# Optimization experiments

Measured on AMD Instinct MI355X. Metric: run time of the kernel, lower is better.

Reference implementation:

```python
import jax, jax.numpy as jnp
import numpy as np

B, N, E, D, H, L = 1, 50000, 800000, 128, 8, 3
HD = D // H
VOCAB = 7000
OUT = 10


def _ln(x, g, b, eps=1e-5):
    m = x.mean(-1, keepdims=True)
    v = ((x - m) ** 2).mean(-1, keepdims=True)
    return (x - m) * jax.lax.rsqrt(v + eps) * g + b


def setup_inputs() -> dict:
    key = jax.random.key(0)
    ks = jax.random.split(key, 40)
    std = 0.02 / np.sqrt(L)

    def w(k, shape):
        return (jax.random.normal(k, shape, jnp.float32) * std)

    inp = {
        "x_idx": jax.random.randint(ks[0], (B, N, 1), 0, VOCAB),
        "edge_index": jax.random.randint(ks[1], (2, E), 0, B * N),
        "emb": jax.random.normal(ks[2], (VOCAB, D), jnp.float32) * 0.02,
        # per-layer params stacked on leading L axis; linears stored [in, out]
        "Wq": w(ks[3], (L, D, D)), "bq": jnp.zeros((L, D), jnp.float32),
        "Wk": w(ks[4], (L, D, D)), "bk": jnp.zeros((L, D), jnp.float32),
        "Wv": w(ks[5], (L, D, D)), "bv": jnp.zeros((L, D), jnp.float32),
        "Wo": w(ks[6], (L, D, D)), "bo": jnp.zeros((L, D), jnp.float32),
        "g1": jnp.ones((L, D), jnp.float32), "be1": jnp.zeros((L, D), jnp.float32),
        "Wf1": w(ks[7], (L, D, 2 * D)), "bf1": jnp.zeros((L, 2 * D), jnp.float32),
        "Wf2": w(ks[8], (L, 2 * D, D)), "bf2": jnp.zeros((L, D), jnp.float32),
        "g2": jnp.ones((L, D), jnp.float32), "be2": jnp.zeros((L, D), jnp.float32),
        # MLPReadout: D -> D/2 -> D/4 -> OUT
        "mW0": w(ks[9], (D, D // 2)), "mb0": jnp.zeros((D // 2,), jnp.float32),
        "mW1": w(ks[10], (D // 2, D // 4)), "mb1": jnp.zeros((D // 4,), jnp.float32),
        "mW2": w(ks[11], (D // 4, OUT)), "mb2": jnp.zeros((OUT,), jnp.float32),
    }
    return inp


def reference(x_idx, edge_index, emb, Wq, bq, Wk, bk, Wv, bv, Wo, bo,
              g1, be1, Wf1, bf1, Wf2, bf2, g2, be2,
              mW0, mb0, mW1, mb1, mW2, mb2):
    # node embedding: sum over feature-index axis -> [B, N, D]
    x = emb[x_idx].sum(axis=-2)
    e0, e1 = edge_index[0], edge_index[1]
    scale = jnp.sqrt(jnp.float32(HD))

    for l in range(L):
        h = x
        hf = h.reshape(B * N, D)
        q = (hf @ Wq[l] + bq[l]).reshape(B * N, H, HD)
        k = (hf @ Wk[l] + bk[l]).reshape(B * N, H, HD)
        v = (hf @ Wv[l] + bv[l]).reshape(B * N, H, HD)
        # edge-indexed gather-mul-exp  [E, H, 1]
        score = jnp.clip(jnp.sum(k[e0] * q[e1], axis=-1, keepdims=True) / scale,
                         -5.0, 5.0)
        score = jnp.exp(score)
        msg = v[e0] * score                                    # [E, H, HD]
        wV = jax.ops.segment_sum(msg, e1, num_segments=B * N)  # [B*N, H, HD]
        Z = jax.ops.segment_sum(score, e1, num_segments=B * N) # [B*N, H, 1]
        attn = (wV / (Z + 1e-6)).reshape(B, N, D)
        y = attn @ Wo[l] + bo[l]
        x = _ln(h + y, g1[l], be1[l])
        # note: FFN input is y (attention output), per the original code
        y2 = jnp.maximum(y @ Wf1[l] + bf1[l], 0.0) @ Wf2[l] + bf2[l]
        x = _ln(x + y2, g2[l], be2[l])

    out = x.mean(axis=1)  # [B, D]
    out = jnp.maximum(out @ mW0 + mb0, 0.0)
    out = jnp.maximum(out @ mW1 + mb1, 0.0)
    return out @ mW2 + mb2  # [B, OUT]
```

## Files before the change

### kernel.cpp

```cpp
#include <hip/hip_runtime.h>
#include <hip/hip_bf16.h>

#define N_NODES 50000
#define N_EDGES 800000
#define DIM 128
#define NLAYERS 3

typedef short bf16x8 __attribute__((ext_vector_type(8)));
typedef float floatx4 __attribute__((ext_vector_type(4)));
typedef float floatx2 __attribute__((ext_vector_type(2)));

__device__ __forceinline__ unsigned short f2bf(float f) {
  unsigned int u = __builtin_bit_cast(unsigned int, f);
  return (unsigned short)((u + 0x7FFFu + ((u >> 16) & 1u)) >> 16);
}
__device__ __forceinline__ float bf2f(unsigned short h) {
  return __builtin_bit_cast(float, (unsigned int)h << 16);
}
__device__ __forceinline__ float2 bf2f2(unsigned int u) {
  float lo = __builtin_bit_cast(float, u << 16);
  float hi = __builtin_bit_cast(float, u & 0xFFFF0000u);
  return make_float2(lo, hi);
}

__global__ __launch_bounds__(256) void embed_kernel(
    const int* __restrict__ idx, const float* __restrict__ emb,
    unsigned short* __restrict__ xb)
{
  int gid = blockIdx.x * 256 + threadIdx.x;
  int n = gid >> 5;
  int c = (gid & 31) << 2;
  if (n >= N_NODES) return;
  int e = idx[n];
  float4 val = *(const float4*)(emb + (size_t)e * DIM + c);
  ushort4 pk;
  pk.x = f2bf(val.x); pk.y = f2bf(val.y); pk.z = f2bf(val.z); pk.w = f2bf(val.w);
  *(ushort4*)(xb + (size_t)n * DIM + c) = pk;
}

__global__ __launch_bounds__(256) void hist_kernel(
    const int* __restrict__ e1, int* __restrict__ counts,
    int* __restrict__ rank)
{
  int i = blockIdx.x * 256 + threadIdx.x;
  if (i < N_EDGES) rank[i] = atomicAdd(&counts[e1[i]], 1);
}

__global__ __launch_bounds__(256) void scan_local(
    const int* __restrict__ counts, int* __restrict__ offsets,
    int* __restrict__ bsums)
{
  __shared__ int buf[256];
  int t = threadIdx.x;
  int i = blockIdx.x * 256 + t;
  int v = (i < N_NODES) ? counts[i] : 0;
  buf[t] = v;
  __syncthreads();
  int s = v;
#pragma unroll
  for (int off = 1; off < 256; off <<= 1) {
    int t2 = (t >= off) ? buf[t - off] : 0;
    __syncthreads();
    s += t2;
    buf[t] = s;
    __syncthreads();
  }
  if (i < N_NODES) offsets[i] = s - v;
  if (t == 255) bsums[blockIdx.x] = s;
}

__global__ void scan_bsums(int* __restrict__ bsums, int nblk)
{
  __shared__ int buf[256];
  int t = threadIdx.x;
  int v = (t < nblk) ? bsums[t] : 0;
  buf[t] = v;
  __syncthreads();
  int s = v;
#pragma unroll
  for (int off = 1; off < 256; off <<= 1) {
    int t2 = (t >= off) ? buf[t - off] : 0;
    __syncthreads();
    s += t2;
    buf[t] = s;
    __syncthreads();
  }
  if (t < nblk) bsums[t] = s - v;
}

__global__ __launch_bounds__(256) void scan_add(
    int* __restrict__ offsets, const int* __restrict__ bsums)
{
  int i = blockIdx.x * 256 + threadIdx.x;
  if (i < N_NODES) offsets[i] += bsums[blockIdx.x];
  if (i == 0) offsets[N_NODES] = N_EDGES;
}

__global__ __launch_bounds__(256) void scatter_kernel(
    const int* __restrict__ e0, const int* __restrict__ e1,
    const int* __restrict__ offsets, const int* __restrict__ rank,
    int* __restrict__ csr)
{
  int i = blockIdx.x * 256 + threadIdx.x;
  if (i >= N_EDGES) return;
  csr[offsets[e1[i]] + rank[i]] = e0[i];
}

__global__ __launch_bounds__(256) void prep_all(
    const float* __restrict__ Wq, const float* __restrict__ Wk,
    const float* __restrict__ Wv, const float* __restrict__ Wo,
    const float* __restrict__ Wf1, const float* __restrict__ Wf2,
    unsigned short* __restrict__ wqkv, unsigned short* __restrict__ wo,
    unsigned short* __restrict__ wf1, unsigned short* __restrict__ wf2)
{
  int g = blockIdx.x * 256 + threadIdx.x;
  if (g < 18432) {
    int srcId = g / 6144; int rem = g - srcId * 6144;
    const float* W = (srcId == 0) ? Wq : (srcId == 1) ? Wk : Wv;
    int l = rem / 2048; int r2 = rem & 2047; int kq = r2 >> 7; int n = r2 & 127;
    const float* Wl = W + (size_t)l * 128 * 128;
    unsigned short* base = wqkv + (size_t)l * 128 * 384 + (size_t)(kq * 384 + srcId * 128 + n) * 8;
#pragma unroll
    for (int j = 0; j < 8; j++)
      base[j] = f2bf(Wl[(size_t)(kq * 8 + j) * 128 + n]);
    return;
  }
  g -= 18432;
  if (g < 6144) {
    int l = g / 2048; int r2 = g & 2047; int kq = r2 >> 7; int n = r2 & 127;
    const float* Wl = Wo + (size_t)l * 128 * 128;
    unsigned short* base = wo + (size_t)l * 128 * 128 + (size_t)(kq * 128 + n) * 8;
#pragma unroll
    for (int j = 0; j < 8; j++)
      base[j] = f2bf(Wl[(size_t)(kq * 8 + j) * 128 + n]);
    return;
  }
  g -= 6144;
  if (g < 12288) {
    int l = g / 4096; int r2 = g & 4095; int kq = r2 >> 8; int n = r2 & 255;
    const float* Wl = Wf1 + (size_t)l * 128 * 256;
    unsigned short* base = wf1 + (size_t)l * 128 * 256 + (size_t)(kq * 256 + n) * 8;
#pragma unroll
    for (int j = 0; j < 8; j++)
      base[j] = f2bf(Wl[(size_t)(kq * 8 + j) * 256 + n]);
    return;
  }
  g -= 12288;
  if (g < 12288) {
    int l = g / 4096; int r2 = g & 4095; int kq = r2 >> 7; int n = r2 & 127;
    const float* Wl = Wf2 + (size_t)l * 256 * 128;
    unsigned short* base = wf2 + (size_t)l * 256 * 128 + (size_t)(kq * 128 + n) * 8;
#pragma unroll
    for (int j = 0; j < 8; j++)
      base[j] = f2bf(Wl[(size_t)(kq * 8 + j) * 128 + n]);
  }
}

#define LSTR 136

__global__ __launch_bounds__(256) void qkv0_kernel(
    const unsigned short* __restrict__ xb,
    const unsigned short* __restrict__ wqkv,
    const float* __restrict__ bq, const float* __restrict__ bk,
    const float* __restrict__ bv,
    unsigned short* __restrict__ qkv, int nrows)
{
  __shared__ unsigned short XR[64 * LSTR];
  int tid = threadIdx.x;
  int wave = tid >> 6, lane = tid & 63;
  int quad = lane >> 4, l16 = lane & 15;
  int rbase = blockIdx.x * 64;
  int wrow = wave * 16;
  int rowg = min(rbase + wrow + l16, nrows - 1);
  int lrow_v = (wrow + l16) * LSTR + quad * 8;
  bool wr = (rbase + wrow + l16 < nrows);

  bf16x8 avQ[4];
  {
    const unsigned short* arow = xb + (size_t)rowg * 128 + quad * 8;
#pragma unroll
    for (int kb = 0; kb < 4; kb++)
      avQ[kb] = *(const bf16x8*)(arow + kb * 32);
  }
#pragma unroll
  for (int c = 0; c < 3; c++) {
    floatx4 accQ[8];
#pragma unroll
    for (int ct = 0; ct < 8; ct++) accQ[ct] = (floatx4)(0.f);
#pragma unroll
    for (int kb = 0; kb < 4; kb++) {
      int kq = kb * 4 + quad;
      bf16x8 bh[8];
#pragma unroll
      for (int ct = 0; ct < 8; ct++)
        bh[ct] = *(const bf16x8*)&wqkv[(size_t)(kq * 384 + c * 128 + ct * 16 + l16) * 8];
#pragma unroll
      for (int ct = 0; ct < 8; ct++)
        accQ[ct] = __builtin_amdgcn_mfma_f32_16x16x32_bf16(avQ[kb], bh[ct], accQ[ct], 0, 0, 0);
    }
    const float* bias = (c == 0) ? bq : (c == 1) ? bk : bv;
#pragma unroll
    for (int ct = 0; ct < 8; ct++) {
      float bvv = bias[ct * 16 + l16];
#pragma unroll
      for (int i = 0; i < 4; i++)
        XR[(wrow + quad * 4 + i) * LSTR + ct * 16 + l16] = f2bf(accQ[ct][i] + bvv);
    }
    if (wr) {
      if (c == 0) {
#pragma unroll
        for (int kb = 0; kb < 4; kb++)
          *(bf16x8*)&qkv[(size_t)(rbase + wrow + l16) * 256 + kb * 32 + quad * 8] =
              *(bf16x8*)&XR[lrow_v + kb * 32];
      } else {
#pragma unroll
        for (int kb = 0; kb < 4; kb++) {
          bf16x8 w = *(bf16x8*)&XR[lrow_v + kb * 32];
          int p0 = __builtin_amdgcn_cvt_pk_fp8_f32(
              bf2f((unsigned short)w[0]) * 8.f, bf2f((unsigned short)w[1]) * 8.f, 0, false);
          int p1 = __builtin_amdgcn_cvt_pk_fp8_f32(
              bf2f((unsigned short)w[2]) * 8.f, bf2f((unsigned short)w[3]) * 8.f, 0, false);
          int p2 = __builtin_amdgcn_cvt_pk_fp8_f32(
              bf2f((unsigned short)w[4]) * 8.f, bf2f((unsigned short)w[5]) * 8.f, 0, false);
          int p3 = __builtin_amdgcn_cvt_pk_fp8_f32(
              bf2f((unsigned short)w[6]) * 8.f, bf2f((unsigned short)w[7]) * 8.f, 0, false);
          int2 st;
          st.x = (p0 & 0xffff) | (p1 << 16);
          st.y = (p2 & 0xffff) | (p3 << 16);
          *(int2*)&qkv[(size_t)(rbase + wrow + l16) * 256 + 128 + (c - 1) * 64 +
                       kb * 16 + quad * 4] = st;
        }
      }
    }
  }
}

__global__ __launch_bounds__(256) void chain1_kernel(
    const unsigned short* __restrict__ a,
    const unsigned short* __restrict__ xb,
    unsigned short* __restrict__ xr,
    unsigned short* __restrict__ ffh,
    const unsigned short* __restrict__ wo, const float* __restrict__ bo,
    const float* __restrict__ g1, const float* __restrict__ be1,
    const unsigned short* __restrict__ wf1, const float* __restrict__ bf1,
    int nrows)
{
  __shared__ unsigned short Y[64 * LSTR];
  __shared__ unsigned short F[64 * LSTR];
  int tid = threadIdx.x;
  int wave = tid >> 6, lane = tid & 63;
  int quad = lane >> 4, l16 = lane & 15;
  int rbase = blockIdx.x * 64;
  int wrow = wave * 16;
  int rowg = min(rbase + wrow + l16, nrows - 1);
  int lrow_v = (wrow + l16) * LSTR + quad * 8;

#pragma unroll
  for (int kb = 0; kb < 4; kb++)
    *(bf16x8*)&F[lrow_v + kb * 32] =
        *(const bf16x8*)&xb[(size_t)rowg * 128 + kb * 32 + quad * 8];

  floatx4 accO[8];
#pragma unroll
  for (int cc = 0; cc < 8; cc++) accO[cc] = (floatx4)(0.f);
  {
    const unsigned short* arow = a + (size_t)rowg * 128 + quad * 8;
#pragma unroll
    for (int kb = 0; kb < 4; kb++) {
      bf16x8 av = *(const bf16x8*)(arow + kb * 32);
      int kq = kb * 4 + quad;
      bf16x8 bh[8];
#pragma unroll
      for (int cc = 0; cc < 8; cc++)
        bh[cc] = *(const bf16x8*)&wo[(size_t)(kq * 128 + cc * 16 + l16) * 8];
#pragma unroll
      for (int cc = 0; cc < 8; cc++)
        accO[cc] = __builtin_amdgcn_mfma_f32_16x16x32_bf16(av, bh[cc], accO[cc], 0, 0, 0);
    }
  }

  {
    float biasO[8], g1v[8], b1v[8];
#pragma unroll
    for (int cc = 0; cc < 8; cc++) {
      int col = cc * 16 + l16;
      biasO[cc] = bo[col]; g1v[cc] = g1[col]; b1v[cc] = be1[col];
    }
#pragma unroll
    for (int i = 0; i < 4; i++) {
      int lrow = wrow + quad * 4 + i;
      float t[8]; float s = 0.f;
#pragma unroll
      for (int cc = 0; cc < 8; cc++) {
        float yv = accO[cc][i] + biasO[cc];
        Y[lrow * LSTR + cc * 16 + l16] = f2bf(yv);
        t[cc] = yv + bf2f(F[lrow * LSTR + cc * 16 + l16]);
        s += t[cc];
      }
      s += __shfl_xor(s, 1); s += __shfl_xor(s, 2);
      s += __shfl_xor(s, 4); s += __shfl_xor(s, 8);
      float mean = s * (1.f / 128.f);
      float vv = 0.f;
#pragma unroll
      for (int cc = 0; cc < 8; cc++) { float d = t[cc] - mean; vv += d * d; }
      vv += __shfl_xor(vv, 1); vv += __shfl_xor(vv, 2);
      vv += __shfl_xor(vv, 4); vv += __shfl_xor(vv, 8);
      float inv = rsqrtf(vv * (1.f / 128.f) + 1e-5f);
#pragma unroll
      for (int cc = 0; cc < 8; cc++)
        F[lrow * LSTR + cc * 16 + l16] =
            f2bf((t[cc] - mean) * inv * g1v[cc] + b1v[cc]);
    }
  }
  if (rbase + wrow + l16 < nrows) {
#pragma unroll
    for (int kb = 0; kb < 4; kb++)
      *(bf16x8*)&xr[(size_t)(rbase + wrow + l16) * 128 + kb * 32 + quad * 8] =
          *(bf16x8*)&F[lrow_v + kb * 32];
  }

  bf16x8 avY[4];
#pragma unroll
  for (int kb = 0; kb < 4; kb++)
    avY[kb] = *(bf16x8*)&Y[lrow_v + kb * 32];
#pragma unroll
  for (int h = 0; h < 2; h++) {
    floatx4 accF[8];
#pragma unroll
    for (int cc = 0; cc < 8; cc++) accF[cc] = (floatx4)(0.f);
#pragma unroll
    for (int kb = 0; kb < 4; kb++) {
      int kq = kb * 4 + quad;
      bf16x8 bh[8];
#pragma unroll
      for (int cc = 0; cc < 8; cc++)
        bh[cc] = *(const bf16x8*)&wf1[(size_t)(kq * 256 + h * 128 + cc * 16 + l16) * 8];
#pragma unroll
      for (int cc = 0; cc < 8; cc++)
        accF[cc] = __builtin_amdgcn_mfma_f32_16x16x32_bf16(avY[kb], bh[cc], accF[cc], 0, 0, 0);
    }
#pragma unroll
    for (int i = 0; i < 4; i++) {
      int lrow = wrow + quad * 4 + i;
#pragma unroll
      for (int cc = 0; cc < 8; cc++)
        F[lrow * LSTR + cc * 16 + l16] =
            f2bf(fmaxf(accF[cc][i] + bf1[h * 128 + cc * 16 + l16], 0.f));
    }
    if (rbase + wrow + l16 < nrows) {
#pragma unroll
      for (int kb = 0; kb < 4; kb++)
        *(bf16x8*)&ffh[(size_t)(rbase + wrow + l16) * 256 + h * 128 + kb * 32 + quad * 8] =
            *(bf16x8*)&F[lrow_v + kb * 32];
    }
  }
}

template<bool LAST>
__global__ __launch_bounds__(256) void chain2_kernel(
    const unsigned short* __restrict__ ffh,
    const unsigned short* __restrict__ xr,
    unsigned short* __restrict__ xb,
    unsigned short* __restrict__ qkv,
    const unsigned short* __restrict__ wf2, const float* __restrict__ bf2,
    const float* __restrict__ g2, const float* __restrict__ be2,
    const unsigned short* __restrict__ wqkv,
    const float* __restrict__ bq, const float* __restrict__ bk,
    const float* __restrict__ bv, int nrows)
{
  __shared__ unsigned short Y[64 * LSTR];
  __shared__ unsigned short XR[64 * LSTR];
  int tid = threadIdx.x;
  int wave = tid >> 6, lane = tid & 63;
  int quad = lane >> 4, l16 = lane & 15;
  int rbase = blockIdx.x * 64;
  int wrow = wave * 16;
  int rowg = min(rbase + wrow + l16, nrows - 1);
  int lrow_v = (wrow + l16) * LSTR + quad * 8;
  bool wr = (rbase + wrow + l16 < nrows);

#pragma unroll
  for (int kb = 0; kb < 4; kb++)
    *(bf16x8*)&XR[lrow_v + kb * 32] =
        *(const bf16x8*)&xr[(size_t)rowg * 128 + kb * 32 + quad * 8];

  floatx4 acc2[8];
#pragma unroll
  for (int cc = 0; cc < 8; cc++) acc2[cc] = (floatx4)(0.f);
  {
    const unsigned short* arow = ffh + (size_t)rowg * 256 + quad * 8;
#pragma unroll
    for (int h = 0; h < 2; h++) {
#pragma unroll
      for (int kb = 0; kb < 4; kb++) {
        bf16x8 av = *(const bf16x8*)(arow + h * 128 + kb * 32);
        int kq = h * 16 + kb * 4 + quad;
        bf16x8 bh[8];
#pragma unroll
        for (int cc = 0; cc < 8; cc++)
          bh[cc] = *(const bf16x8*)&wf2[(size_t)(kq * 128 + cc * 16 + l16) * 8];
#pragma unroll
        for (int cc = 0; cc < 8; cc++)
          acc2[cc] = __builtin_amdgcn_mfma_f32_16x16x32_bf16(av, bh[cc], acc2[cc], 0, 0, 0);
      }
    }
  }

  {
    float bias2[8], g2v[8], b2v[8];
#pragma unroll
    for (int cc = 0; cc < 8; cc++) {
      int col = cc * 16 + l16;
      bias2[cc] = bf2[col]; g2v[cc] = g2[col]; b2v[cc] = be2[col];
    }
#pragma unroll
    for (int i = 0; i < 4; i++) {
      int lrow = wrow + quad * 4 + i;
      float t[8]; float s = 0.f;
#pragma unroll
      for (int cc = 0; cc < 8; cc++) {
        t[cc] = acc2[cc][i] + bias2[cc] + bf2f(XR[lrow * LSTR + cc * 16 + l16]);
        s += t[cc];
      }
      s += __shfl_xor(s, 1); s += __shfl_xor(s, 2);
      s += __shfl_xor(s, 4); s += __shfl_xor(s, 8);
      float mean = s * (1.f / 128.f);
      float vv = 0.f;
#pragma unroll
      for (int cc = 0; cc < 8; cc++) { float d = t[cc] - mean; vv += d * d; }
      vv += __shfl_xor(vv, 1); vv += __shfl_xor(vv, 2);
      vv += __shfl_xor(vv, 4); vv += __shfl_xor(vv, 8);
      float inv = rsqrtf(vv * (1.f / 128.f) + 1e-5f);
#pragma unroll
      for (int cc = 0; cc < 8; cc++)
        Y[lrow * LSTR + cc * 16 + l16] =
            f2bf((t[cc] - mean) * inv * g2v[cc] + b2v[cc]);
    }
  }
  if (wr) {
#pragma unroll
    for (int kb = 0; kb < 4; kb++)
      *(bf16x8*)&xb[(size_t)(rbase + wrow + l16) * 128 + kb * 32 + quad * 8] =
          *(bf16x8*)&Y[lrow_v + kb * 32];
  }

  if (!LAST) {
    bf16x8 avQ[4];
#pragma unroll
    for (int kb = 0; kb < 4; kb++)
      avQ[kb] = *(bf16x8*)&Y[lrow_v + kb * 32];
#pragma unroll
    for (int c = 0; c < 3; c++) {
      floatx4 accQ[8];
#pragma unroll
      for (int ct = 0; ct < 8; ct++) accQ[ct] = (floatx4)(0.f);
#pragma unroll
      for (int kb = 0; kb < 4; kb++) {
        int kq = kb * 4 + quad;
        bf16x8 bh[8];
#pragma unroll
        for (int ct = 0; ct < 8; ct++)
          bh[ct] = *(const bf16x8*)&wqkv[(size_t)(kq * 384 + c * 128 + ct * 16 + l16) * 8];
#pragma unroll
        for (int ct = 0; ct < 8; ct++)
          accQ[ct] = __builtin_amdgcn_mfma_f32_16x16x32_bf16(avQ[kb], bh[ct], accQ[ct], 0, 0, 0);
      }
      const float* bias = (c == 0) ? bq : (c == 1) ? bk : bv;
#pragma unroll
      for (int ct = 0; ct < 8; ct++) {
        float bvv = bias[ct * 16 + l16];
#pragma unroll
        for (int i = 0; i < 4; i++)
          XR[(wrow + quad * 4 + i) * LSTR + ct * 16 + l16] = f2bf(accQ[ct][i] + bvv);
      }
      if (wr) {
        if (c == 0) {
#pragma unroll
          for (int kb = 0; kb < 4; kb++)
            *(bf16x8*)&qkv[(size_t)(rbase + wrow + l16) * 256 + kb * 32 + quad * 8] =
                *(bf16x8*)&XR[lrow_v + kb * 32];
        } else {
#pragma unroll
          for (int kb = 0; kb < 4; kb++) {
            bf16x8 w = *(bf16x8*)&XR[lrow_v + kb * 32];
            int p0 = __builtin_amdgcn_cvt_pk_fp8_f32(
                bf2f((unsigned short)w[0]) * 8.f, bf2f((unsigned short)w[1]) * 8.f, 0, false);
            int p1 = __builtin_amdgcn_cvt_pk_fp8_f32(
                bf2f((unsigned short)w[2]) * 8.f, bf2f((unsigned short)w[3]) * 8.f, 0, false);
            int p2 = __builtin_amdgcn_cvt_pk_fp8_f32(
                bf2f((unsigned short)w[4]) * 8.f, bf2f((unsigned short)w[5]) * 8.f, 0, false);
            int p3 = __builtin_amdgcn_cvt_pk_fp8_f32(
                bf2f((unsigned short)w[6]) * 8.f, bf2f((unsigned short)w[7]) * 8.f, 0, false);
            int2 st;
            st.x = (p0 & 0xffff) | (p1 << 16);
            st.y = (p2 & 0xffff) | (p3 << 16);
            *(int2*)&qkv[(size_t)(rbase + wrow + l16) * 256 + 128 + (c - 1) * 64 +
                         kb * 16 + quad * 4] = st;
          }
        }
      }
    }
  }
}
#undef LSTR

#define ATTN_C8 0.04508422003f
#define ATTN_L  7.21347520444f
__device__ __forceinline__ float edge_score8(float p) {
  float t = fminf(fmaxf(p * ATTN_C8, -ATTN_L), ATTN_L);
  return __builtin_amdgcn_exp2f(t);
}
__global__ __launch_bounds__(256) void attn_kernel(
    const unsigned short* __restrict__ qkv,
    const int* __restrict__ offsets, const int* __restrict__ csr,
    unsigned short* __restrict__ attn)
{
  int node = blockIdx.x * 8 + (threadIdx.x >> 5);
  int l32 = threadIdx.x & 31;
  if (node >= N_NODES) return;
  float q0, q1, q2v, q3;
  {
    ushort4 qu = *(const ushort4*)(qkv + (size_t)node * 256 + l32 * 4);
    q0 = bf2f(qu.x); q1 = bf2f(qu.y); q2v = bf2f(qu.z); q3 = bf2f(qu.w);
  }
  const unsigned short* kb8 = qkv + 128 + l32 * 2;
  const unsigned short* vb8 = qkv + 192 + l32 * 2;
  float w0 = 0.f, w1 = 0.f, w2 = 0.f, w3 = 0.f, z = 0.f;
  int j = offsets[node], end = offsets[node + 1];
  for (; j + 4 <= end; j += 4) {
    int s[4];
#pragma unroll
    for (int u = 0; u < 4; u++) s[u] = csr[j + u] << 8;
    unsigned int ku[4], vu[4];
#pragma unroll
    for (int u = 0; u < 4; u++) {
      ku[u] = *(const unsigned int*)(kb8 + s[u]);
      vu[u] = *(const unsigned int*)(vb8 + s[u]);
    }
    float p[4];
#pragma unroll
    for (int u = 0; u < 4; u++) {
      floatx2 ka = __builtin_amdgcn_cvt_pk_f32_fp8((int)ku[u], false);
      floatx2 kc = __builtin_amdgcn_cvt_pk_f32_fp8((int)ku[u], true);
      p[u] = fmaf(ka[0], q0, fmaf(ka[1], q1, fmaf(kc[0], q2v, kc[1] * q3)));
    }
#pragma unroll
    for (int u = 0; u < 4; u++) p[u] += __shfl_xor(p[u], 1);
#pragma unroll
    for (int u = 0; u < 4; u++) p[u] += __shfl_xor(p[u], 2);
#pragma unroll
    for (int u = 0; u < 4; u++) {
      float sc = edge_score8(p[u]);
      floatx2 va = __builtin_amdgcn_cvt_pk_f32_fp8((int)vu[u], false);
      floatx2 vc = __builtin_amdgcn_cvt_pk_f32_fp8((int)vu[u], true);
      w0 = fmaf(sc, va[0], w0); w1 = fmaf(sc, va[1], w1);
      w2 = fmaf(sc, vc[0], w2); w3 = fmaf(sc, vc[1], w3);
      z += sc;
    }
  }
  for (; j < end; ++j) {
    int s = csr[j] << 8;
    unsigned int ku = *(const unsigned int*)(kb8 + s);
    unsigned int vu = *(const unsigned int*)(vb8 + s);
    floatx2 ka = __builtin_amdgcn_cvt_pk_f32_fp8((int)ku, false);
    floatx2 kc = __builtin_amdgcn_cvt_pk_f32_fp8((int)ku, true);
    float p = fmaf(ka[0], q0, fmaf(ka[1], q1, fmaf(kc[0], q2v, kc[1] * q3)));
    p += __shfl_xor(p, 1); p += __shfl_xor(p, 2);
    float sc = edge_score8(p);
    floatx2 va = __builtin_amdgcn_cvt_pk_f32_fp8((int)vu, false);
    floatx2 vc = __builtin_amdgcn_cvt_pk_f32_fp8((int)vu, true);
    w0 = fmaf(sc, va[0], w0); w1 = fmaf(sc, va[1], w1);
    w2 = fmaf(sc, vc[0], w2); w3 = fmaf(sc, vc[1], w3);
    z += sc;
  }
  float inv = 1.f / (8.f * z + 8e-6f);
  ushort4 pk;
  pk.x = f2bf(w0 * inv); pk.y = f2bf(w1 * inv);
  pk.z = f2bf(w2 * inv); pk.w = f2bf(w3 * inv);
  *(ushort4*)(attn + (size_t)node * DIM + l32 * 4) = pk;
}

#define CM_BLOCKS 128
__global__ __launch_bounds__(256) void colsum_partial(
    const unsigned short* __restrict__ xb, float* __restrict__ partial)
{
  int cg = threadIdx.x & 15;
  int ro = threadIdx.x >> 4;
  int rows = (N_NODES + CM_BLOCKS - 1) / CM_BLOCKS;
  int r0 = blockIdx.x * rows;
  int r1 = min(r0 + rows, N_NODES);
  float acc[8];
#pragma unroll
  for (int j = 0; j < 8; j++) acc[j] = 0.f;
  int r = r0 + ro;
  for (; r + 48 < r1; r += 64) {
    bf16x8 v0 = *(const bf16x8*)&xb[(size_t)r * 128 + cg * 8];
    bf16x8 v1 = *(const bf16x8*)&xb[(size_t)(r + 16) * 128 + cg * 8];
    bf16x8 v2 = *(const bf16x8*)&xb[(size_t)(r + 32) * 128 + cg * 8];
    bf16x8 v3 = *(const bf16x8*)&xb[(size_t)(r + 48) * 128 + cg * 8];
#pragma unroll
    for (int j = 0; j < 8; j++)
      acc[j] += (bf2f((unsigned short)v0[j]) + bf2f((unsigned short)v1[j])) +
                (bf2f((unsigned short)v2[j]) + bf2f((unsigned short)v3[j]));
  }
  for (; r < r1; r += 16) {
    bf16x8 v = *(const bf16x8*)&xb[(size_t)r * 128 + cg * 8];
#pragma unroll
    for (int j = 0; j < 8; j++) acc[j] += bf2f((unsigned short)v[j]);
  }
  __shared__ float s[16 * 128];
#pragma unroll
  for (int j = 0; j < 8; j++) s[ro * 128 + cg * 8 + j] = acc[j];
  __syncthreads();
#pragma unroll
  for (int step = 8; step >= 1; step >>= 1) {
    if (ro < step) {
#pragma unroll
      for (int j = 0; j < 8; j++)
        s[ro * 128 + cg * 8 + j] += s[(ro + step) * 128 + cg * 8 + j];
    }
    __syncthreads();
  }
  if (ro < 2) {
    int c = ro * 64 + cg * 4;
    *(float4*)&partial[(size_t)blockIdx.x * 128 + c] = *(float4*)&s[c];
  }
}

__global__ void readout_kernel(
    const float* __restrict__ partial,
    const float* __restrict__ mW0, const float* __restrict__ mb0,
    const float* __restrict__ mW1, const float* __restrict__ mb1,
    const float* __restrict__ mW2, const float* __restrict__ mb2,
    float* __restrict__ out)
{
  __shared__ float sx[128], h0[64], h1[32];
  int t = threadIdx.x;
  {
    float s0 = 0.f, s1 = 0.f, s2 = 0.f, s3 = 0.f;
#pragma unroll 2
    for (int p = 0; p < CM_BLOCKS; p += 4) {
      s0 += partial[(size_t)p * 128 + t];
      s1 += partial[(size_t)(p + 1) * 128 + t];
      s2 += partial[(size_t)(p + 2) * 128 + t];
      s3 += partial[(size_t)(p + 3) * 128 + t];
    }
    sx[t] = ((s0 + s1) + (s2 + s3)) * (1.f / (float)N_NODES);
  }
  __syncthreads();
  if (t < 64) {
    float a = mb0[t];
    for (int i = 0; i < 128; i++) a = fmaf(sx[i], mW0[i * 64 + t], a);
    h0[t] = fmaxf(a, 0.f);
  }
  __syncthreads();
  if (t < 32) {
    float a = mb1[t];
    for (int i = 0; i < 64; i++) a = fmaf(h0[i], mW1[i * 32 + t], a);
    h1[t] = fmaxf(a, 0.f);
  }
  __syncthreads();
  if (t < 10) {
    float a = mb2[t];
    for (int i = 0; i < 32; i++) a = fmaf(h1[i], mW2[i * 10 + t], a);
    out[t] = a;
  }
}

extern "C" void kernel_launch(void* const* d_in, const int* in_sizes, int n_in,
                              void* d_out, int out_size, void* d_ws, size_t ws_size,
                              hipStream_t stream) {
  const int*   x_idx = (const int*)d_in[0];
  const int*   eidx  = (const int*)d_in[1];
  const float* emb   = (const float*)d_in[2];
  const float* Wq = (const float*)d_in[3];  const float* bq = (const float*)d_in[4];
  const float* Wk = (const float*)d_in[5];  const float* bk = (const float*)d_in[6];
  const float* Wv = (const float*)d_in[7];  const float* bv = (const float*)d_in[8];
  const float* Wo = (const float*)d_in[9];  const float* bo = (const float*)d_in[10];
  const float* g1 = (const float*)d_in[11]; const float* be1 = (const float*)d_in[12];
  const float* Wf1 = (const float*)d_in[13]; const float* bf1 = (const float*)d_in[14];
  const float* Wf2 = (const float*)d_in[15]; const float* bf2 = (const float*)d_in[16];
  const float* g2 = (const float*)d_in[17]; const float* be2 = (const float*)d_in[18];
  const float* mW0 = (const float*)d_in[19]; const float* mb0 = (const float*)d_in[20];
  const float* mW1 = (const float*)d_in[21]; const float* mb1 = (const float*)d_in[22];
  const float* mW2 = (const float*)d_in[23]; const float* mb2 = (const float*)d_in[24];
  float* out = (float*)d_out;

  const size_t NX = (size_t)N_NODES * DIM;
  unsigned short* xb  = (unsigned short*)d_ws;
  unsigned short* qkv = xb + NX;
  unsigned short* a   = qkv + (size_t)N_NODES * 256;
  unsigned short* xr  = a + NX;
  unsigned short* ffh = xr + NX;

  unsigned short* wqkv_p = ffh + (size_t)N_NODES * 256;
  unsigned short* wo_p   = wqkv_p + 3 * 128 * 384;
  unsigned short* wf1_p  = wo_p   + 3 * 128 * 128;
  unsigned short* wf2_p  = wf1_p  + 3 * 128 * 256;
  unsigned short* wend   = wf2_p  + 3 * 256 * 128;

  int* counts    = (int*)wend;
  float* partial = (float*)(counts + N_NODES);
  int* offsets   = (int*)(partial + CM_BLOCKS * 128);
  int* bsums     = offsets + N_NODES + 1;
  int* csr       = bsums + 256;
  int* rank      = csr + N_EDGES;

  const int* e0 = eidx;
  const int* e1 = eidx + N_EDGES;

  hipMemsetAsync(counts, 0, N_NODES * sizeof(int), stream);

  prep_all<<<192, 256, 0, stream>>>(Wq, Wk, Wv, Wo, Wf1, Wf2,
                                    wqkv_p, wo_p, wf1_p, wf2_p);

  embed_kernel<<<(N_NODES * 32 + 255) / 256, 256, 0, stream>>>(x_idx, emb, xb);
  hist_kernel<<<(N_EDGES + 255) / 256, 256, 0, stream>>>(e1, counts, rank);
  int nblk = (N_NODES + 255) / 256;
  scan_local<<<nblk, 256, 0, stream>>>(counts, offsets, bsums);
  scan_bsums<<<1, 256, 0, stream>>>(bsums, nblk);
  scan_add<<<nblk, 256, 0, stream>>>(offsets, bsums);
  scatter_kernel<<<(N_EDGES + 255) / 256, 256, 0, stream>>>(e0, e1, offsets, rank, csr);

  int gc = (N_NODES + 63) / 64;
  int nb8 = (N_NODES + 7) / 8;

  qkv0_kernel<<<gc, 256, 0, stream>>>(xb, wqkv_p, bq, bk, bv, qkv, N_NODES);

  for (int l = 0; l < NLAYERS; ++l) {
    const unsigned short* wo_l   = wo_p   + (size_t)l * 128 * 128;
    const unsigned short* wf1_l  = wf1_p  + (size_t)l * 128 * 256;
    const unsigned short* wf2_l  = wf2_p  + (size_t)l * 256 * 128;
    const unsigned short* wqkv_n = wqkv_p + (size_t)(l + 1) * 128 * 384;
    const float* bo_l  = bo  + (size_t)l * DIM;
    const float* g1_l  = g1  + (size_t)l * DIM;
    const float* be1_l = be1 + (size_t)l * DIM;
    const float* bf1_l = bf1 + (size_t)l * 2 * DIM;
    const float* bf2_l = bf2 + (size_t)l * DIM;
    const float* g2_l  = g2  + (size_t)l * DIM;
    const float* be2_l = be2 + (size_t)l * DIM;

    attn_kernel<<<nb8, 256, 0, stream>>>(qkv, offsets, csr, a);
    chain1_kernel<<<gc, 256, 0, stream>>>(
        a, xb, xr, ffh, wo_l, bo_l, g1_l, be1_l, wf1_l, bf1_l, N_NODES);
    if (l < NLAYERS - 1) {
      chain2_kernel<false><<<gc, 256, 0, stream>>>(
          ffh, xr, xb, qkv, wf2_l, bf2_l, g2_l, be2_l, wqkv_n,
          bq + (size_t)(l + 1) * DIM, bk + (size_t)(l + 1) * DIM,
          bv + (size_t)(l + 1) * DIM, N_NODES);
    } else {
      chain2_kernel<true><<<gc, 256, 0, stream>>>(
          ffh, xr, xb, qkv, wf2_l, bf2_l, g2_l, be2_l, wqkv_p,
          bq, bk, bv, N_NODES);
    }
  }

  colsum_partial<<<CM_BLOCKS, 256, 0, stream>>>(xb, partial);
  readout_kernel<<<1, 128, 0, stream>>>(partial, mW0, mb0, mW1, mb1, mW2, mb2, out);
}
```

Measured before the change: 485.6 us.

## Fuse chain1 and chain2 into single per-layer node MLP kernel

Merges the attention-output/LN1/FFN1 kernel with the FFN2/LN2/next-QKV kernel so the LN1 result stays in registers and the FFN hidden activations stay in shared memory. This removes the global round-trips through the xr and ffh buffers and one kernel launch per layer. In exchange the fused kernel holds more live registers (the x1 values plus the accumulators), which may lower occupancy.

```diff
diff --git a/kernel.cpp b/kernel.cpp
--- a/kernel.cpp
+++ b/kernel.cpp
@@ -16,11 +16,6 @@
 }
 __device__ __forceinline__ float bf2f(unsigned short h) {
   return __builtin_bit_cast(float, (unsigned int)h << 16);
-}
-__device__ __forceinline__ float2 bf2f2(unsigned int u) {
-  float lo = __builtin_bit_cast(float, u << 16);
-  float hi = __builtin_bit_cast(float, u & 0xFFFF0000u);
-  return make_float2(lo, hi);
 }
 
 __global__ __launch_bounds__(256) void embed_kernel(
@@ -235,15 +230,19 @@
   }
 }
 
-__global__ __launch_bounds__(256) void chain1_kernel(
+template<bool LAST>
+__global__ __launch_bounds__(256) void chainM_kernel(
     const unsigned short* __restrict__ a,
-    const unsigned short* __restrict__ xb,
-    unsigned short* __restrict__ xr,
-    unsigned short* __restrict__ ffh,
+    unsigned short* __restrict__ xb,
+    unsigned short* __restrict__ qkv,
     const unsigned short* __restrict__ wo, const float* __restrict__ bo,
     const float* __restrict__ g1, const float* __restrict__ be1,
     const unsigned short* __restrict__ wf1, const float* __restrict__ bf1,
-    int nrows)
+    const unsigned short* __restrict__ wf2, const float* __restrict__ bf2,
+    const float* __restrict__ g2, const float* __restrict__ be2,
+    const unsigned short* __restrict__ wqkv,
+    const float* __restrict__ bq, const float* __restrict__ bk,
+    const float* __restrict__ bv, int nrows)
 {
   __shared__ unsigned short Y[64 * LSTR];
   __shared__ unsigned short F[64 * LSTR];
@@ -254,6 +253,7 @@
   int wrow = wave * 16;
   int rowg = min(rbase + wrow + l16, nrows - 1);
   int lrow_v = (wrow + l16) * LSTR + quad * 8;
+  bool wr = (rbase + wrow + l16 < nrows);
 
 #pragma unroll
   for (int kb = 0; kb < 4; kb++)
@@ -279,6 +279,7 @@
     }
   }
 
+  float x1v[8][4];
   {
     float biasO[8], g1v[8], b1v[8];
 #pragma unroll
@@ -308,21 +309,17 @@
       float inv = rsqrtf(vv * (1.f / 128.f) + 1e-5f);
 #pragma unroll
       for (int cc = 0; cc < 8; cc++)
-        F[lrow * LSTR + cc * 16 + l16] =
-            f2bf((t[cc] - mean) * inv * g1v[cc] + b1v[cc]);
-    }
-  }
-  if (rbase + wrow + l16 < nrows) {
-#pragma unroll
-    for (int kb = 0; kb < 4; kb++)
-      *(bf16x8*)&xr[(size_t)(rbase + wrow + l16) * 128 + kb * 32 + quad * 8] =
-          *(bf16x8*)&F[lrow_v + kb * 32];
+        x1v[cc][i] = bf2f(f2bf((t[cc] - mean) * inv * g1v[cc] + b1v[cc]));
+    }
   }
 
   bf16x8 avY[4];
 #pragma unroll
   for (int kb = 0; kb < 4; kb++)
     avY[kb] = *(bf16x8*)&Y[lrow_v + kb * 32];
+  floatx4 acc2[8];
+#pragma unroll
+  for (int cc = 0; cc < 8; cc++) acc2[cc] = (floatx4)(0.f);
 #pragma unroll
   for (int h = 0; h < 2; h++) {
     floatx4 accF[8];
@@ -347,62 +344,17 @@
         F[lrow * LSTR + cc * 16 + l16] =
             f2bf(fmaxf(accF[cc][i] + bf1[h * 128 + cc * 16 + l16], 0.f));
     }
-    if (rbase + wrow + l16 < nrows) {
-#pragma unroll
-      for (int kb = 0; kb < 4; kb++)
-        *(bf16x8*)&ffh[(size_t)(rbase + wrow + l16) * 256 + h * 128 + kb * 32 + quad * 8] =
-            *(bf16x8*)&F[lrow_v + kb * 32];
-    }
-  }
-}
-
-template<bool LAST>
-__global__ __launch_bounds__(256) void chain2_kernel(
-    const unsigned short* __restrict__ ffh,
-    const unsigned short* __restrict__ xr,
-    unsigned short* __restrict__ xb,
-    unsigned short* __restrict__ qkv,
-    const unsigned short* __restrict__ wf2, const float* __restrict__ bf2,
-    const float* __restrict__ g2, const float* __restrict__ be2,
-    const unsigned short* __restrict__ wqkv,
-    const float* __restrict__ bq, const float* __restrict__ bk,
-    const float* __restrict__ bv, int nrows)
-{
-  __shared__ unsigned short Y[64 * LSTR];
-  __shared__ unsigned short XR[64 * LSTR];
-  int tid = threadIdx.x;
-  int wave = tid >> 6, lane = tid & 63;
-  int quad = lane >> 4, l16 = lane & 15;
-  int rbase = blockIdx.x * 64;
-  int wrow = wave * 16;
-  int rowg = min(rbase + wrow + l16, nrows - 1);
-  int lrow_v = (wrow + l16) * LSTR + quad * 8;
-  bool wr = (rbase + wrow + l16 < nrows);
-
-#pragma unroll
-  for (int kb = 0; kb < 4; kb++)
-    *(bf16x8*)&XR[lrow_v + kb * 32] =
-        *(const bf16x8*)&xr[(size_t)rowg * 128 + kb * 32 + quad * 8];
-
-  floatx4 acc2[8];
-#pragma unroll
-  for (int cc = 0; cc < 8; cc++) acc2[cc] = (floatx4)(0.f);
-  {
-    const unsigned short* arow = ffh + (size_t)rowg * 256 + quad * 8;
-#pragma unroll
-    for (int h = 0; h < 2; h++) {
-#pragma unroll
-      for (int kb = 0; kb < 4; kb++) {
-        bf16x8 av = *(const bf16x8*)(arow + h * 128 + kb * 32);
-        int kq = h * 16 + kb * 4 + quad;
-        bf16x8 bh[8];
-#pragma unroll
-        for (int cc = 0; cc < 8; cc++)
-          bh[cc] = *(const bf16x8*)&wf2[(size_t)(kq * 128 + cc * 16 + l16) * 8];
-#pragma unroll
-        for (int cc = 0; cc < 8; cc++)
-          acc2[cc] = __builtin_amdgcn_mfma_f32_16x16x32_bf16(av, bh[cc], acc2[cc], 0, 0, 0);
-      }
+#pragma unroll
+    for (int kb = 0; kb < 4; kb++) {
+      bf16x8 avF = *(bf16x8*)&F[lrow_v + kb * 32];
+      int kq = h * 16 + kb * 4 + quad;
+      bf16x8 bh[8];
+#pragma unroll
+      for (int cc = 0; cc < 8; cc++)
+        bh[cc] = *(const bf16x8*)&wf2[(size_t)(kq * 128 + cc * 16 + l16) * 8];
+#pragma unroll
+      for (int cc = 0; cc < 8; cc++)
+        acc2[cc] = __builtin_amdgcn_mfma_f32_16x16x32_bf16(avF, bh[cc], acc2[cc], 0, 0, 0);
     }
   }
 
@@ -419,7 +371,7 @@
       float t[8]; float s = 0.f;
 #pragma unroll
       for (int cc = 0; cc < 8; cc++) {
-        t[cc] = acc2[cc][i] + bias2[cc] + bf2f(XR[lrow * LSTR + cc * 16 + l16]);
+        t[cc] = acc2[cc][i] + bias2[cc] + x1v[cc][i];
         s += t[cc];
       }
       s += __shfl_xor(s, 1); s += __shfl_xor(s, 2);
@@ -471,18 +423,18 @@
         float bvv = bias[ct * 16 + l16];
 #pragma unroll
         for (int i = 0; i < 4; i++)
-          XR[(wrow + quad * 4 + i) * LSTR + ct * 16 + l16] = f2bf(accQ[ct][i] + bvv);
+          F[(wrow + quad * 4 + i) * LSTR + ct * 16 + l16] = f2bf(accQ[ct][i] + bvv);
       }
       if (wr) {
         if (c == 0) {
 #pragma unroll
           for (int kb = 0; kb < 4; kb++)
             *(bf16x8*)&qkv[(size_t)(rbase + wrow + l16) * 256 + kb * 32 + quad * 8] =
-                *(bf16x8*)&XR[lrow_v + kb * 32];
+                *(bf16x8*)&F[lrow_v + kb * 32];
         } else {
 #pragma unroll
           for (int kb = 0; kb < 4; kb++) {
-            bf16x8 w = *(bf16x8*)&XR[lrow_v + kb * 32];
+            bf16x8 w = *(bf16x8*)&F[lrow_v + kb * 32];
             int p0 = __builtin_amdgcn_cvt_pk_fp8_f32(
                 bf2f((unsigned short)w[0]) * 8.f, bf2f((unsigned short)w[1]) * 8.f, 0, false);
             int p1 = __builtin_amdgcn_cvt_pk_fp8_f32(
@@ -690,10 +642,8 @@
   unsigned short* xb  = (unsigned short*)d_ws;
   unsigned short* qkv = xb + NX;
   unsigned short* a   = qkv + (size_t)N_NODES * 256;
-  unsigned short* xr  = a + NX;
-  unsigned short* ffh = xr + NX;
-
-  unsigned short* wqkv_p = ffh + (size_t)N_NODES * 256;
+
+  unsigned short* wqkv_p = a + NX;
   unsigned short* wo_p   = wqkv_p + 3 * 128 * 384;
   unsigned short* wf1_p  = wo_p   + 3 * 128 * 128;
   unsigned short* wf2_p  = wf1_p  + 3 * 128 * 256;
@@ -741,17 +691,16 @@
     const float* be2_l = be2 + (size_t)l * DIM;
 
     attn_kernel<<<nb8, 256, 0, stream>>>(qkv, offsets, csr, a);
-    chain1_kernel<<<gc, 256, 0, stream>>>(
-        a, xb, xr, ffh, wo_l, bo_l, g1_l, be1_l, wf1_l, bf1_l, N_NODES);
     if (l < NLAYERS - 1) {
-      chain2_kernel<false><<<gc, 256, 0, stream>>>(
-          ffh, xr, xb, qkv, wf2_l, bf2_l, g2_l, be2_l, wqkv_n,
+      chainM_kernel<false><<<gc, 256, 0, stream>>>(
+          a, xb, qkv, wo_l, bo_l, g1_l, be1_l, wf1_l, bf1_l, wf2_l, bf2_l,
+          g2_l, be2_l, wqkv_n,
           bq + (size_t)(l + 1) * DIM, bk + (size_t)(l + 1) * DIM,
           bv + (size_t)(l + 1) * DIM, N_NODES);
     } else {
-      chain2_kernel<true><<<gc, 256, 0, stream>>>(
-          ffh, xr, xb, qkv, wf2_l, bf2_l, g2_l, be2_l, wqkv_p,
-          bq, bk, bv, N_NODES);
+      chainM_kernel<true><<<gc, 256, 0, stream>>>(
+          a, xb, qkv, wo_l, bo_l, g1_l, be1_l, wf1_l, bf1_l, wf2_l, bf2_l,
+          g2_l, be2_l, wqkv_p, bq, bk, bv, N_NODES);
     }
   }
 
```

Result: faster. 442.9 us, median of 2 (-8.8%).
